# Optimization experiments

Hardware: AMD Instinct MI355X
Metric: run time of the kernel (lower is better)

The kernel has to match this reference:

```python
import jax, jax.numpy as jnp
import numpy as np

B, H, S, DK, DV = 2, 16, 2048, 128, 128


def setup_inputs() -> dict:
    key = jax.random.key(0)
    kq, kk, kv = jax.random.split(key, 3)
    query = jax.random.normal(kq, (B, H, S, DK), dtype=jnp.float32)
    k_ = jax.random.normal(kk, (B, H, S, DK), dtype=jnp.float32)
    value = jax.random.normal(kv, (B, H, S, DV), dtype=jnp.float32)
    # causal mask: True = masked out (upper triangle above diagonal)
    causal = ~jnp.tril(jnp.ones((S, S), dtype=bool))
    mask = jnp.broadcast_to(causal[None, None, :, :], (B, 1, S, S))
    return {"query": query, "key": k_, "value": value, "mask": mask}


def reference(query, key, value, mask):
    d_k = query.shape[-1]
    # scores: (B, H, Sq, Sk)
    scores = jnp.einsum("bhqd,bhkd->bhqk", query, key) / jnp.sqrt(jnp.float32(d_k))
    scores = jnp.where(mask, -jnp.inf, scores)
    attention_weights = jax.nn.softmax(scores, axis=-1)
    # dropout p=0.0 (eval) -> identity
    output = jnp.einsum("bhqk,bhkv->bhqv", attention_weights, value)
    return (output, attention_weights)
```

## Files before the change

kernel.cpp:

```cpp
#include <hip/hip_runtime.h>
#include <hip/hip_bf16.h>


typedef __attribute__((ext_vector_type(4))) float  f32x4;
typedef __attribute__((ext_vector_type(8))) short  short8;

#define S_LEN 2048
#define DKK   128
#define QBLK  64
#define KBLK  64
#define NBH   32

__device__ __forceinline__ short f2bf(float f) {
    unsigned u = __builtin_bit_cast(unsigned, f);
    u += 0x7FFF + ((u >> 16) & 1);
    return (short)(u >> 16);
}

__device__ __forceinline__ void g2l16(const void* g, void* l) {
    __builtin_amdgcn_global_load_lds(
        (const __attribute__((address_space(1))) unsigned int*)g,
        (__attribute__((address_space(3))) unsigned int*)l, 16, 0, 0);
}


__global__ __launch_bounds__(256) void conv_q(const float* __restrict__ Q,
                                              short* __restrict__ Qs) {
    const float SC = 0.08838834764831845f * 1.4426950408889634f;
    const int NCH = NBH * S_LEN * (DKK / 8);
    for (int g = blockIdx.x * 256 + threadIdx.x; g < NCH; g += gridDim.x * 256) {
        const float* p = Q + (size_t)g * 8;
        f32x4 a = *(const f32x4*)p;
        f32x4 b = *(const f32x4*)(p + 4);
        short8 r;
        #pragma unroll
        for (int j = 0; j < 4; ++j) {
            r[j]     = f2bf(a[j] * SC);
            r[4 + j] = f2bf(b[j] * SC);
        }
        *(short8*)(Qs + (size_t)g * 8) = r;
    }
}

__global__ __launch_bounds__(256) void conv_k(const float* __restrict__ K,
                                              short* __restrict__ Kb) {
    const int NCH = NBH * S_LEN * (DKK / 8);
    for (int g = blockIdx.x * 256 + threadIdx.x; g < NCH; g += gridDim.x * 256) {
        const int row = g >> 4;
        const int c   = g & 15;
        const float* p = K + (size_t)row * DKK + c * 8;
        f32x4 a = *(const f32x4*)p;
        f32x4 b = *(const f32x4*)(p + 4);
        short8 r;
        #pragma unroll
        for (int j = 0; j < 4; ++j) {
            r[j]     = f2bf(a[j]);
            r[4 + j] = f2bf(b[j]);
        }
        *(short8*)(Kb + (size_t)row * DKK + (size_t)(c ^ (row & 7)) * 8) = r;
    }
}

__global__ __launch_bounds__(256) void conv_vt(const float* __restrict__ V,
                                               short* __restrict__ VT) {
    __shared__ short tile[64][130];
    const int bh = blockIdx.x >> 5;
    const int kt = blockIdx.x & 31;
    const float* Vb = V + ((size_t)bh * S_LEN + kt * 64) * DKK;
    const int t  = threadIdx.x;
    const int k8 = t >> 5, d0 = (t & 31) * 4;
    #pragma unroll
    for (int it = 0; it < 8; ++it) {
        int k = it * 8 + k8;
        f32x4 v = *(const f32x4*)(Vb + (size_t)k * DKK + d0);
        #pragma unroll
        for (int j = 0; j < 4; ++j) tile[k][d0 + j] = f2bf(v[j]);
    }
    __syncthreads();
    const int d = t >> 1, half = t & 1;
    short* outb = VT + (size_t)bh * DKK * S_LEN + (size_t)d * S_LEN + kt * 64;
    #pragma unroll
    for (int cc = 0; cc < 4; ++cc) {
        short8 r;
        #pragma unroll
        for (int j = 0; j < 8; ++j) r[j] = tile[half * 32 + cc * 8 + j][d];
        int cp = (half * 4 + cc) ^ (d & 7);
        *(short8*)(outb + cp * 8) = r;
    }
}


__global__ __launch_bounds__(256) void attn_main(
    const short* __restrict__ Qs, const short* __restrict__ Kb,
    const short* __restrict__ VT, float* __restrict__ O,
    float* __restrict__ W)
{
    __shared__ __align__(16) short kT[2][KBLK * DKK];
    __shared__ __align__(16) short vtT[2][DKK * KBLK];
    __shared__ __align__(16) short pT[4][16 * KBLK];

    const int tid  = threadIdx.x;
    const int lane = tid & 63;
    const int w    = tid >> 6;
    const int lg   = lane >> 4;
    const int lr   = lane & 15;

    const int bh = (blockIdx.x & 7) * 4 + ((blockIdx.x >> 3) & 3);
    const int qt = 31 - (blockIdx.x >> 5);
    const int q0 = qt * QBLK;
    const int qbase = q0 + w * 16;
    const int kend = q0 + QBLK;
    const int ntk  = qt + 1;

    const short* Qb  = Qs + (size_t)bh * S_LEN * DKK;
    const short* Kbh = Kb + (size_t)bh * S_LEN * DKK;
    const short* VTb = VT + (size_t)bh * DKK * S_LEN;
    float* Ob = O + (size_t)bh * S_LEN * DKK;
    float* Wb = W + (size_t)bh * S_LEN * S_LEN;

    short8 qf[4];
    #pragma unroll
    for (int ds = 0; ds < 4; ++ds)
        qf[ds] = *(const short8*)(Qb + (size_t)(qbase + lr) * DKK + lg * 8 + ds * 32);

    auto stage_k = [&](int buf, int kt_) {
        const char* gk = (const char*)(Kbh + (size_t)kt_ * KBLK * DKK);
        char* lk = (char*)kT[buf];
        #pragma unroll
        for (int i = 0; i < 4; ++i)
            g2l16(gk + i * 4096 + tid * 16, lk + i * 4096 + w * 1024);
    };
    auto stage_v = [&](int buf, int kt_) {
        const char* gv = (const char*)VTb + (size_t)kt_ * KBLK * 2;
        char* lv = (char*)vtT[buf];
        #pragma unroll
        for (int i = 0; i < 4; ++i) {
            int L = i * 4096 + tid * 16;
            g2l16(gv + (size_t)(L >> 7) * 4096 + (L & 127),
                  lv + i * 4096 + w * 1024);
        }
    };

    float lsum[4] = {0.f, 0.f, 0.f, 0.f};
    int cur = 0;
    stage_k(0, 0);
    for (int kt_ = 0; kt_ < ntk; ++kt_) {
        __syncthreads();
        if (kt_ + 1 < ntk) stage_k(cur ^ 1, kt_ + 1);
        const int k0 = kt_ * KBLK;
        const char* kBc = (const char*)kT[cur];
        #pragma unroll
        for (int t = 0; t < 4; ++t) {
            f32x4 d = {0.f, 0.f, 0.f, 0.f};
            __builtin_amdgcn_s_setprio(1);
            #pragma unroll
            for (int ds = 0; ds < 4; ++ds) {
                const int krow = t * 16 + lr;
                const int off  = (krow * 256 + ds * 64 + lg * 16) ^ ((krow & 7) << 4);
                d = __builtin_amdgcn_mfma_f32_16x16x32_bf16(
                        qf[ds], *(const short8*)(kBc + off), d, 0, 0, 0);
            }
            __builtin_amdgcn_s_setprio(0);
            const int kg = k0 + t * 16 + lr;
            #pragma unroll
            for (int r = 0; r < 4; ++r) {
                const int qg = qbase + lg * 4 + r;
                if (kg <= qg) lsum[r] += exp2f(d[r]);
            }
        }
        cur ^= 1;
    }
    #pragma unroll
    for (int r = 0; r < 4; ++r) {
        float s = lsum[r];
        s += __shfl_xor(s, 1);
        s += __shfl_xor(s, 2);
        s += __shfl_xor(s, 4);
        s += __shfl_xor(s, 8);
        lsum[r] = 1.0f / s;
    }

    f32x4 acc[8];
    #pragma unroll
    for (int i = 0; i < 8; ++i) acc[i] = (f32x4){0.f, 0.f, 0.f, 0.f};

    __syncthreads();
    cur = 0;
    stage_k(0, 0);
    stage_v(0, 0);
    for (int kt_ = 0; kt_ < ntk; ++kt_) {
        __syncthreads();
        if (kt_ + 1 < ntk) { stage_k(cur ^ 1, kt_ + 1); stage_v(cur ^ 1, kt_ + 1); }
        const int k0 = kt_ * KBLK;
        const char* kBc = (const char*)kT[cur];
        const char* vBc = (const char*)vtT[cur];
        char* pBc = (char*)pT[w];

        #pragma unroll
        for (int t = 0; t < 4; ++t) {
            f32x4 d = {0.f, 0.f, 0.f, 0.f};
            __builtin_amdgcn_s_setprio(1);
            #pragma unroll
            for (int ds = 0; ds < 4; ++ds) {
                const int krow = t * 16 + lr;
                const int off  = (krow * 256 + ds * 64 + lg * 16) ^ ((krow & 7) << 4);
                d = __builtin_amdgcn_mfma_f32_16x16x32_bf16(
                        qf[ds], *(const short8*)(kBc + off), d, 0, 0, 0);
            }
            __builtin_amdgcn_s_setprio(0);
            const int kg = k0 + t * 16 + lr;
            #pragma unroll
            for (int r = 0; r < 4; ++r) {
                const int qg = qbase + lg * 4 + r;
                const float p = (kg <= qg) ? exp2f(d[r]) * lsum[r] : 0.f;
                Wb[(size_t)qg * S_LEN + kg] = p;
                const int qr  = lg * 4 + r;
                const int off = (qr * 128 + (t * 16 + lr) * 2) ^ ((qr & 7) << 4);
                *(short*)(pBc + off) = f2bf(p);
            }
        }
        #pragma unroll
        for (int h = 0; h < 2; ++h) {
            const int poff = (lr * 128 + h * 64 + lg * 16) ^ ((lr & 7) << 4);
            short8 pa = *(const short8*)(pBc + poff);
            __builtin_amdgcn_s_setprio(1);
            #pragma unroll
            for (int nt = 0; nt < 8; ++nt) {
                const int dv   = nt * 16 + lr;
                const int voff = (dv * 128 + h * 64 + lg * 16) ^ ((dv & 7) << 4);
                short8 vf = *(const short8*)(vBc + voff);
                acc[nt] = __builtin_amdgcn_mfma_f32_16x16x32_bf16(pa, vf, acc[nt], 0, 0, 0);
            }
            __builtin_amdgcn_s_setprio(0);
        }
        cur ^= 1;
    }

    #pragma unroll
    for (int nt = 0; nt < 8; ++nt)
        #pragma unroll
        for (int r = 0; r < 4; ++r)
            Ob[(size_t)(qbase + lg * 4 + r) * DKK + nt * 16 + lr] = acc[nt][r];

    const int zc = S_LEN - kend;
    if (zc > 0) {
        const int yo = tid >> 2;
        const int xo = tid & 3;
        float* wrow = Wb + (size_t)(q0 + yo) * S_LEN + kend;
        const f32x4 z = {0.f, 0.f, 0.f, 0.f};
        for (int c = xo * 4; c < zc; c += 16)
            *(f32x4*)(wrow + c) = z;
    }
}

extern "C" void kernel_launch(void* const* d_in, const int* in_sizes, int n_in,
                              void* d_out, int out_size, void* d_ws, size_t ws_size,
                              hipStream_t stream) {
    const float* Q = (const float*)d_in[0];
    const float* K = (const float*)d_in[1];
    const float* V = (const float*)d_in[2];
    float* O = (float*)d_out;
    float* W = (float*)d_out + (size_t)NBH * S_LEN * DKK;

    const size_t TEN = (size_t)NBH * S_LEN * DKK;
    short* Qs  = (short*)d_ws;
    short* Kb  = Qs + TEN;
    short* VTw = Kb + TEN;

    conv_q <<<2048, 256, 0, stream>>>(Q, Qs);
    conv_k <<<2048, 256, 0, stream>>>(K, Kb);
    conv_vt<<<1024, 256, 0, stream>>>(V, VTw);
    attn_main<<<1024, 256, 0, stream>>>(Qs, Kb, VTw, O, W);
}
```

Measured before the change: 252.9 us.

## Fuse Q conversion into attention, transpose score MFMA for vectorized W stores

Drops the separate conv_q kernel and instead loads fp32 Q inside attn_main, scaling and converting it to bf16 in registers. The score MFMA operands are swapped so each lane owns one query row and four consecutive keys. This allows 16-byte W stores and 8-byte P stores to LDS, and reduces the row-sum reduction to two shuffles. The first (row-sum) pass now reads K straight from global/L2 instead of double-buffered LDS, removing its barriers but relying on cache hits for K reuse.

```diff
diff --git a/kernel.cpp b/kernel.cpp
--- a/kernel.cpp
+++ b/kernel.cpp
@@ -4,6 +4,7 @@
 
 typedef __attribute__((ext_vector_type(4))) float  f32x4;
 typedef __attribute__((ext_vector_type(8))) short  short8;
+typedef __attribute__((ext_vector_type(4))) short  short4v;
 
 #define S_LEN 2048
 #define DKK   128
@@ -23,24 +24,6 @@
         (__attribute__((address_space(3))) unsigned int*)l, 16, 0, 0);
 }
 
-
-__global__ __launch_bounds__(256) void conv_q(const float* __restrict__ Q,
-                                              short* __restrict__ Qs) {
-    const float SC = 0.08838834764831845f * 1.4426950408889634f;
-    const int NCH = NBH * S_LEN * (DKK / 8);
-    for (int g = blockIdx.x * 256 + threadIdx.x; g < NCH; g += gridDim.x * 256) {
-        const float* p = Q + (size_t)g * 8;
-        f32x4 a = *(const f32x4*)p;
-        f32x4 b = *(const f32x4*)(p + 4);
-        short8 r;
-        #pragma unroll
-        for (int j = 0; j < 4; ++j) {
-            r[j]     = f2bf(a[j] * SC);
-            r[4 + j] = f2bf(b[j] * SC);
-        }
-        *(short8*)(Qs + (size_t)g * 8) = r;
-    }
-}
 
 __global__ __launch_bounds__(256) void conv_k(const float* __restrict__ K,
                                               short* __restrict__ Kb) {
@@ -91,7 +74,7 @@
 
 
 __global__ __launch_bounds__(256) void attn_main(
-    const short* __restrict__ Qs, const short* __restrict__ Kb,
+    const float* __restrict__ Qf, const short* __restrict__ Kb,
     const short* __restrict__ VT, float* __restrict__ O,
     float* __restrict__ W)
 {
@@ -104,6 +87,7 @@
     const int w    = tid >> 6;
     const int lg   = lane >> 4;
     const int lr   = lane & 15;
+    const int s7   = lr & 7;
 
     const int bh = (blockIdx.x & 7) * 4 + ((blockIdx.x >> 3) & 3);
     const int qt = 31 - (blockIdx.x >> 5);
@@ -111,17 +95,30 @@
     const int qbase = q0 + w * 16;
     const int kend = q0 + QBLK;
     const int ntk  = qt + 1;
-
-    const short* Qb  = Qs + (size_t)bh * S_LEN * DKK;
+    const int qg   = qbase + lr;
+
     const short* Kbh = Kb + (size_t)bh * S_LEN * DKK;
     const short* VTb = VT + (size_t)bh * DKK * S_LEN;
     float* Ob = O + (size_t)bh * S_LEN * DKK;
     float* Wb = W + (size_t)bh * S_LEN * S_LEN;
 
+    const float QSCALE = 0.08838834764831845f * 1.4426950408889634f;
     short8 qf[4];
-    #pragma unroll
-    for (int ds = 0; ds < 4; ++ds)
-        qf[ds] = *(const short8*)(Qb + (size_t)(qbase + lr) * DKK + lg * 8 + ds * 32);
+    {
+        const float* qp = Qf + ((size_t)bh * S_LEN + qg) * DKK + lg * 8;
+        #pragma unroll
+        for (int ds = 0; ds < 4; ++ds) {
+            f32x4 a = *(const f32x4*)(qp + ds * 32);
+            f32x4 b = *(const f32x4*)(qp + ds * 32 + 4);
+            short8 r;
+            #pragma unroll
+            for (int j = 0; j < 4; ++j) {
+                r[j]     = f2bf(a[j] * QSCALE);
+                r[4 + j] = f2bf(b[j] * QSCALE);
+            }
+            qf[ds] = r;
+        }
+    }
 
     auto stage_k = [&](int buf, int kt_) {
         const char* gk = (const char*)(Kbh + (size_t)kt_ * KBLK * DKK);
@@ -141,53 +138,41 @@
         }
     };
 
-    float lsum[4] = {0.f, 0.f, 0.f, 0.f};
-    int cur = 0;
-    stage_k(0, 0);
-    for (int kt_ = 0; kt_ < ntk; ++kt_) {
-        __syncthreads();
-        if (kt_ + 1 < ntk) stage_k(cur ^ 1, kt_ + 1);
-        const int k0 = kt_ * KBLK;
-        const char* kBc = (const char*)kT[cur];
-        #pragma unroll
-        for (int t = 0; t < 4; ++t) {
-            f32x4 d = {0.f, 0.f, 0.f, 0.f};
-            __builtin_amdgcn_s_setprio(1);
-            #pragma unroll
-            for (int ds = 0; ds < 4; ++ds) {
-                const int krow = t * 16 + lr;
-                const int off  = (krow * 256 + ds * 64 + lg * 16) ^ ((krow & 7) << 4);
-                d = __builtin_amdgcn_mfma_f32_16x16x32_bf16(
-                        qf[ds], *(const short8*)(kBc + off), d, 0, 0, 0);
-            }
-            __builtin_amdgcn_s_setprio(0);
-            const int kg = k0 + t * 16 + lr;
-            #pragma unroll
-            for (int r = 0; r < 4; ++r) {
-                const int qg = qbase + lg * 4 + r;
-                if (kg <= qg) lsum[r] += exp2f(d[r]);
-            }
-        }
-        cur ^= 1;
-    }
-    #pragma unroll
-    for (int r = 0; r < 4; ++r) {
-        float s = lsum[r];
-        s += __shfl_xor(s, 1);
-        s += __shfl_xor(s, 2);
-        s += __shfl_xor(s, 4);
-        s += __shfl_xor(s, 8);
-        lsum[r] = 1.0f / s;
-    }
-
-    f32x4 acc[8];
-    #pragma unroll
-    for (int i = 0; i < 8; ++i) acc[i] = (f32x4){0.f, 0.f, 0.f, 0.f};
-
-    __syncthreads();
-    cur = 0;
     stage_k(0, 0);
     stage_v(0, 0);
+
+    float lsum = 0.f;
+    {
+        const char* kG = (const char*)Kbh;
+        for (int kt_ = 0; kt_ < ntk; ++kt_) {
+            const int k0 = kt_ * KBLK;
+            #pragma unroll
+            for (int t = 0; t < 4; ++t) {
+                const char* rowp = kG + (size_t)(k0 + 16 * t + lr) * 256;
+                f32x4 d = {0.f, 0.f, 0.f, 0.f};
+                __builtin_amdgcn_s_setprio(1);
+                #pragma unroll
+                for (int ds = 0; ds < 4; ++ds)
+                    d = __builtin_amdgcn_mfma_f32_16x16x32_bf16(
+                            *(const short8*)(rowp + (((lg + ds * 4) ^ s7) * 16)),
+                            qf[ds], d, 0, 0, 0);
+                __builtin_amdgcn_s_setprio(0);
+                const int kb = k0 + 16 * t + lg * 4;
+                #pragma unroll
+                for (int r = 0; r < 4; ++r)
+                    lsum += (kb + r <= qg) ? exp2f(d[r]) : 0.f;
+            }
+        }
+    }
+    lsum += __shfl_xor(lsum, 16);
+    lsum += __shfl_xor(lsum, 32);
+    const float invl = 1.0f / lsum;
+
+    f32x4 acc[8];
+    #pragma unroll
+    for (int i = 0; i < 8; ++i) acc[i] = (f32x4){0.f, 0.f, 0.f, 0.f};
+
+    int cur = 0;
     for (int kt_ = 0; kt_ < ntk; ++kt_) {
         __syncthreads();
         if (kt_ + 1 < ntk) { stage_k(cur ^ 1, kt_ + 1); stage_v(cur ^ 1, kt_ + 1); }
@@ -198,36 +183,37 @@
 
         #pragma unroll
         for (int t = 0; t < 4; ++t) {
+            const int krow = t * 16 + lr;
             f32x4 d = {0.f, 0.f, 0.f, 0.f};
             __builtin_amdgcn_s_setprio(1);
             #pragma unroll
             for (int ds = 0; ds < 4; ++ds) {
-                const int krow = t * 16 + lr;
-                const int off  = (krow * 256 + ds * 64 + lg * 16) ^ ((krow & 7) << 4);
+                const int off = (krow * 256 + ds * 64 + lg * 16) ^ (s7 << 4);
                 d = __builtin_amdgcn_mfma_f32_16x16x32_bf16(
-                        qf[ds], *(const short8*)(kBc + off), d, 0, 0, 0);
+                        *(const short8*)(kBc + off), qf[ds], d, 0, 0, 0);
             }
             __builtin_amdgcn_s_setprio(0);
-            const int kg = k0 + t * 16 + lr;
+            const int kb = k0 + 16 * t + lg * 4;
+            f32x4 pv;
+            short4v pb;
             #pragma unroll
             for (int r = 0; r < 4; ++r) {
-                const int qg = qbase + lg * 4 + r;
-                const float p = (kg <= qg) ? exp2f(d[r]) * lsum[r] : 0.f;
-                Wb[(size_t)qg * S_LEN + kg] = p;
-                const int qr  = lg * 4 + r;
-                const int off = (qr * 128 + (t * 16 + lr) * 2) ^ ((qr & 7) << 4);
-                *(short*)(pBc + off) = f2bf(p);
-            }
+                const float p = (kb + r <= qg) ? exp2f(d[r]) * invl : 0.f;
+                pv[r] = p;
+                pb[r] = f2bf(p);
+            }
+            *(f32x4*)(Wb + (size_t)qg * S_LEN + kb) = pv;
+            const int poff = lr * 128 + (((16 * t + lg * 4) * 2) ^ (s7 << 4));
+            *(short4v*)(pBc + poff) = pb;
         }
         #pragma unroll
         for (int h = 0; h < 2; ++h) {
-            const int poff = (lr * 128 + h * 64 + lg * 16) ^ ((lr & 7) << 4);
+            const int poff = lr * 128 + ((h * 64 + lg * 16) ^ (s7 << 4));
             short8 pa = *(const short8*)(pBc + poff);
             __builtin_amdgcn_s_setprio(1);
             #pragma unroll
             for (int nt = 0; nt < 8; ++nt) {
-                const int dv   = nt * 16 + lr;
-                const int voff = (dv * 128 + h * 64 + lg * 16) ^ ((dv & 7) << 4);
+                const int voff = (nt * 16 + lr) * 128 + ((h * 64 + lg * 16) ^ (s7 << 4));
                 short8 vf = *(const short8*)(vBc + voff);
                 acc[nt] = __builtin_amdgcn_mfma_f32_16x16x32_bf16(pa, vf, acc[nt], 0, 0, 0);
             }
@@ -263,12 +249,10 @@
     float* W = (float*)d_out + (size_t)NBH * S_LEN * DKK;
 
     const size_t TEN = (size_t)NBH * S_LEN * DKK;
-    short* Qs  = (short*)d_ws;
-    short* Kb  = Qs + TEN;
+    short* Kb  = (short*)d_ws;
     short* VTw = Kb + TEN;
 
-    conv_q <<<2048, 256, 0, stream>>>(Q, Qs);
     conv_k <<<2048, 256, 0, stream>>>(K, Kb);
     conv_vt<<<1024, 256, 0, stream>>>(V, VTw);
-    attn_main<<<1024, 256, 0, stream>>>(Qs, Kb, VTw, O, W);
-}
+    attn_main<<<1024, 256, 0, stream>>>(Q, Kb, VTw, O, W);
+}
```

Result: slower. 261.0 us (+3.2%).
